# Kernel optimization log

Measured on AMD Instinct MI355X. Metric: run time of the kernel, lower is better.

The kernel has to match this reference:

```python
import jax, jax.numpy as jnp
import numpy as np


def setup_inputs() -> dict:
    key = jax.random.key(0)
    k1, k2, k3, k4 = jax.random.split(key, 4)
    N, E, F_IN, H, C = 100000, 1600000, 128, 64, 64
    x = jax.random.normal(k1, (N, F_IN), dtype=jnp.float32)
    edge_index = jax.random.randint(k2, (2, E), 0, N, dtype=jnp.int64)
    W1 = jax.random.normal(k3, (F_IN, H), dtype=jnp.float32) / np.sqrt(F_IN)
    b1 = jnp.zeros((H,), dtype=jnp.float32)
    W2 = jax.random.normal(k4, (H, C), dtype=jnp.float32) / np.sqrt(H)
    b2 = jnp.zeros((C,), dtype=jnp.float32)
    return {"x": x, "edge_index": edge_index, "W1": W1, "b1": b1, "W2": W2, "b2": b2}


def reference(x, edge_index, W1, b1, W2, b2):
    N = x.shape[0]
    # add self-loops (PyG GCNConv default)
    loop = jnp.arange(N, dtype=edge_index.dtype)
    src = jnp.concatenate([edge_index[0], loop])
    dst = jnp.concatenate([edge_index[1], loop])
    # symmetric normalization: deg^{-1/2}[src] * deg^{-1/2}[dst], deg over dst
    deg = jax.ops.segment_sum(jnp.ones_like(dst, dtype=x.dtype), dst, num_segments=N)
    dis = jnp.where(deg > 0, jax.lax.rsqrt(deg), 0.0)
    norm = dis[src] * dis[dst]  # [E+N]

    def gcn_conv(h, W, b):
        h = h @ W                                   # [N, out]
        msg = h[src] * norm[:, None]                # [E+N, out] gather
        agg = jax.ops.segment_sum(msg, dst, num_segments=N)  # scatter-add
        return agg + b

    h = jax.nn.relu(gcn_conv(x, W1, b1))
    # dropout inactive in eval mode
    out = gcn_conv(h, W2, b2)
    return jax.nn.log_softmax(out, axis=1)
```

## Files before the change

### kernel.cpp

```cpp
#include <hip/hip_runtime.h>
#include <cstdint>
#include <cstddef>

#define PASSA_EDGES 2048

typedef __attribute__((ext_vector_type(8))) short bf16x8;
typedef __attribute__((ext_vector_type(4))) float f32x4;


__device__ __forceinline__ unsigned short f2bf(float f) {
    unsigned int u = __float_as_uint(f);
    u += 0x7FFFu + ((u >> 16) & 1u);
    return (unsigned short)(u >> 16);
}
__device__ __forceinline__ float bf2f(unsigned short h) {
    return __uint_as_float((unsigned int)h << 16);
}

__device__ __forceinline__ void bf8_acc(uint4 u, float* acc) {
    acc[0] += __uint_as_float(u.x << 16);
    acc[1] += __uint_as_float(u.x & 0xFFFF0000u);
    acc[2] += __uint_as_float(u.y << 16);
    acc[3] += __uint_as_float(u.y & 0xFFFF0000u);
    acc[4] += __uint_as_float(u.z << 16);
    acc[5] += __uint_as_float(u.z & 0xFFFF0000u);
    acc[6] += __uint_as_float(u.w << 16);
    acc[7] += __uint_as_float(u.w & 0xFFFF0000u);
}
__device__ __forceinline__ void bf8_unpack(uint4 u, float* v) {
    v[0] = __uint_as_float(u.x << 16);
    v[1] = __uint_as_float(u.x & 0xFFFF0000u);
    v[2] = __uint_as_float(u.y << 16);
    v[3] = __uint_as_float(u.y & 0xFFFF0000u);
    v[4] = __uint_as_float(u.z << 16);
    v[5] = __uint_as_float(u.z & 0xFFFF0000u);
    v[6] = __uint_as_float(u.w << 16);
    v[7] = __uint_as_float(u.w & 0xFFFF0000u);
}


__global__ __launch_bounds__(256) void passA(const int* __restrict__ src,
                                             const int* __restrict__ dst,
                                             int* __restrict__ bcur,
                                             int2* __restrict__ bbuf, int E,
                                             int CAP, int shift) {
    __shared__ int2 bins[PASSA_EDGES];
    __shared__ int  cnt[256], off[256], cur[256], gbase[256];
    const int t  = threadIdx.x;
    const int e0 = blockIdx.x * PASSA_EDGES;
    const int n  = min(PASSA_EDGES, E - e0);

    cnt[t] = 0;
    __syncthreads();
    for (int i = t; i < n; i += 256) atomicAdd(&cnt[dst[e0 + i] >> shift], 1);
    __syncthreads();

    const int v = cnt[t];
    off[t] = v;
    __syncthreads();
    for (int o = 1; o < 256; o <<= 1) {
        int u = (t >= o) ? off[t - o] : 0;
        __syncthreads();
        off[t] += u;
        __syncthreads();
    }
    const int excl = off[t] - v;
    off[t] = excl;
    cur[t] = excl;
    if (v > 0) gbase[t] = t * CAP + atomicAdd(&bcur[t], v);
    __syncthreads();

    for (int i = t; i < n; i += 256) {
        const int d = dst[e0 + i];
        const int s = src[e0 + i];
        const int p = atomicAdd(&cur[d >> shift], 1);
        bins[p] = make_int2(s, d);
    }
    __syncthreads();

    for (int i = t; i < n; i += 256) {
        const int2 pr = bins[i];
        const int  b  = pr.y >> shift;
        const int  q  = gbase[b] + (i - off[b]);
        if (q < (b + 1) * CAP) bbuf[q] = pr;
    }
}


__global__ __launch_bounds__(256) void hist_dis(const int2* __restrict__ bbuf,
                                                const int* __restrict__ bcur,
                                                int* __restrict__ hist,
                                                int N, int CAP, int shift) {
    __shared__ int cnt[1024];
    const int b     = blockIdx.x;
    const int node0 = b << shift;
    const int nn    = min(1 << shift, N - node0);
    for (int j = threadIdx.x; j < nn; j += 256) cnt[j] = 0;
    __syncthreads();
    const int start = b * CAP;
    const int end   = min(b * CAP + bcur[b], (b + 1) * CAP);
    for (int e = start + threadIdx.x; e < end; e += 256)
        atomicAdd(&cnt[bbuf[e].y - node0], 1);
    __syncthreads();
    for (int j = threadIdx.x; j < nn; j += 256) hist[node0 + j] = cnt[j];
}


__global__ __launch_bounds__(256) void scan_partial(const int* __restrict__ hist,
                                                    int* __restrict__ partials,
                                                    float* __restrict__ dis, int N) {
    __shared__ int red[256];
    const int t    = threadIdx.x;
    const int base = blockIdx.x * 1024 + t * 4;
    int s = 0;
    if (base + 3 < N) {
        int4 v = *(const int4*)&hist[base];
        s = ((v.x + 7) & ~7) + ((v.y + 7) & ~7) + ((v.z + 7) & ~7) + ((v.w + 7) & ~7);
        dis[base]     = rsqrtf((float)(v.x + 1));
        dis[base + 1] = rsqrtf((float)(v.y + 1));
        dis[base + 2] = rsqrtf((float)(v.z + 1));
        dis[base + 3] = rsqrtf((float)(v.w + 1));
    } else {
        for (int i = 0; i < 4; i++)
            if (base + i < N) {
                int c = hist[base + i];
                s += (c + 7) & ~7;
                dis[base + i] = rsqrtf((float)(c + 1));
            }
    }
    red[t] = s;
    __syncthreads();
    for (int off = 128; off; off >>= 1) {
        if (t < off) red[t] += red[t + off];
        __syncthreads();
    }
    if (t == 0) partials[blockIdx.x] = red[0];
}

__global__ __launch_bounds__(256) void scan_offsets(int* __restrict__ partials, int NB) {
    __shared__ int tmp[256];
    const int t = threadIdx.x;
    int v = (t < NB) ? partials[t] : 0;
    tmp[t] = v;
    __syncthreads();
    for (int off = 1; off < 256; off <<= 1) {
        int u = (t >= off) ? tmp[t - off] : 0;
        __syncthreads();
        tmp[t] += u;
        __syncthreads();
    }
    if (t < NB) partials[t] = tmp[t] - v;
}

__global__ __launch_bounds__(256) void scan_apply(const int* __restrict__ hist,
                                                  const int* __restrict__ partials,
                                                  int* __restrict__ ptr, int N) {
    __shared__ int tsum[256];
    const int t    = threadIdx.x;
    const int base = blockIdx.x * 1024 + t * 4;
    int v[4];
    int s = 0;
    for (int i = 0; i < 4; i++) {
        int c = (base + i < N) ? hist[base + i] : 0;
        v[i]  = (c + 7) & ~7;
        s += v[i];
    }
    tsum[t] = s;
    __syncthreads();
    for (int off = 1; off < 256; off <<= 1) {
        int u = (t >= off) ? tsum[t - off] : 0;
        __syncthreads();
        tsum[t] += u;
        __syncthreads();
    }
    int run = partials[blockIdx.x] + tsum[t] - s;
    for (int i = 0; i < 4; i++) {
        if (base + i < N) {
            ptr[base + i] = run;
            run += v[i];
        }
    }
    if (base <= N - 1 && N - 1 < base + 4) ptr[N] = run;
}


__global__ __launch_bounds__(256) void passB(const int2* __restrict__ bbuf,
                                             const int* __restrict__ bcur,
                                             const int* __restrict__ ptr,
                                             int* __restrict__ csr,
                                             int N, int CAP, int shift) {
    __shared__ int lcur[1024];
    const int b     = blockIdx.x;
    const int node0 = b << shift;
    const int nn    = min(1 << shift, N - node0);
    for (int j = threadIdx.x; j < nn; j += 256) lcur[j] = ptr[node0 + j];
    __syncthreads();

    const int start = b * CAP;
    const int end   = min(b * CAP + bcur[b], (b + 1) * CAP);
    for (int e = start + threadIdx.x; e < end; e += 256) {
        const int2 pr = bbuf[e];
        const int  p  = atomicAdd(&lcur[pr.y - node0], 1);
        csr[p] = pr.x;
    }
    __syncthreads();

    for (int j = threadIdx.x; j < nn; j += 256) {
        const int t1 = ptr[node0 + j + 1];
        for (int p = lcur[j]; p < t1; ++p) csr[p] = N;
    }
}


__global__ __launch_bounds__(256) void prep_wfrag(const float* __restrict__ W1,
                                                  const float* __restrict__ W2,
                                                  unsigned short* __restrict__ whi1,
                                                  unsigned short* __restrict__ wlo1,
                                                  unsigned short* __restrict__ whi2,
                                                  unsigned short* __restrict__ wlo2) {
    for (int e = threadIdx.x; e < 128 * 64; e += 256) {
        const int blk = e >> 9, l = (e >> 3) & 63, j = e & 7;
        const int k = (blk >> 2) * 32 + (l >> 4) * 8 + j;
        const int n = (blk & 3) * 16 + (l & 15);
        const float v = W1[k * 64 + n];
        const unsigned short h = f2bf(v);
        whi1[e] = h;
        wlo1[e] = f2bf(v - bf2f(h));
    }
    for (int e = threadIdx.x; e < 64 * 64; e += 256) {
        const int blk = e >> 9, l = (e >> 3) & 63, j = e & 7;
        const int k = (blk >> 2) * 32 + (l >> 4) * 8 + j;
        const int n = (blk & 3) * 16 + (l & 15);
        const float v = W2[k * 64 + n];
        const unsigned short h = f2bf(v);
        whi2[e] = h;
        wlo2[e] = f2bf(v - bf2f(h));
    }
}


template <int K>
__global__ __launch_bounds__(256) void gemm_mfma(const float* __restrict__ X,
                                                 const unsigned short* __restrict__ whi,
                                                 const unsigned short* __restrict__ wlo,
                                                 const float* __restrict__ dis,
                                                 unsigned short* __restrict__ Yb, int N) {
    constexpr int LDX = K + 4;
    __shared__ float xs[64 * LDX];
    const int tid  = threadIdx.x;
    const int row0 = blockIdx.x * 64;

#pragma unroll
    for (int i = 0; i < (64 * K) / 1024; ++i) {
        const int fidx = i * 1024 + tid * 4;
        const int r = fidx / K, c = fidx % K;
        const float4 v = *(const float4*)(X + (size_t)min(row0 + r, N - 1) * K + c);
        *(float4*)&xs[r * LDX + c] = v;
    }
    __syncthreads();

    const int w = tid >> 6, l = tid & 63;
    const int m = l & 15, kg = l >> 4;

    f32x4 acc[4] = {};
    const float* xrow = &xs[(w * 16 + m) * LDX];

#pragma unroll
    for (int s = 0; s < K / 32; ++s) {
        const float4 a0 = *(const float4*)(xrow + s * 32 + kg * 8);
        const float4 a1 = *(const float4*)(xrow + s * 32 + kg * 8 + 4);
        const float av[8] = {a0.x, a0.y, a0.z, a0.w, a1.x, a1.y, a1.z, a1.w};
        bf16x8 ahi, alo;
#pragma unroll
        for (int j = 0; j < 8; ++j) {
            const unsigned short h = f2bf(av[j]);
            ahi[j] = (short)h;
            alo[j] = (short)f2bf(av[j] - bf2f(h));
        }
#pragma unroll
        for (int nt = 0; nt < 4; ++nt) {
            const bf16x8 bh = *(const bf16x8*)&whi[(s * 4 + nt) * 512 + l * 8];
            const bf16x8 bl = *(const bf16x8*)&wlo[(s * 4 + nt) * 512 + l * 8];
            acc[nt] = __builtin_amdgcn_mfma_f32_16x16x32_bf16(ahi, bh, acc[nt], 0, 0, 0);
            acc[nt] = __builtin_amdgcn_mfma_f32_16x16x32_bf16(alo, bh, acc[nt], 0, 0, 0);
            acc[nt] = __builtin_amdgcn_mfma_f32_16x16x32_bf16(ahi, bl, acc[nt], 0, 0, 0);
        }
    }

    float dv[4];
#pragma unroll
    for (int r = 0; r < 4; ++r)
        dv[r] = dis[min(row0 + w * 16 + kg * 4 + r, N - 1)];

#pragma unroll
    for (int nt = 0; nt < 4; ++nt)
#pragma unroll
        for (int r = 0; r < 4; ++r) {
            const int row = row0 + w * 16 + kg * 4 + r;
            if (row < N) Yb[(size_t)row * 64 + nt * 16 + m] = f2bf(acc[nt][r] * dv[r]);
        }
}


__device__ __forceinline__ void gather8i(const unsigned short* __restrict__ B,
                                         const int* __restrict__ csr,
                                         int s0, int iters, int co, float* acc) {
    const int4* cs = (const int4*)(csr + s0);
    int4 c0 = make_int4(0, 0, 0, 0), c1 = c0;
    if (iters > 0) { c0 = cs[0]; c1 = cs[1]; }
    for (int it = 0; it < iters; ++it) {
        const int nb = min(it + 1, iters - 1) * 2;
        int4 n0 = cs[nb], n1 = cs[nb + 1];
        uint4 u0 = *(const uint4*)&B[(size_t)c0.x * 64 + co * 8];
        uint4 u1 = *(const uint4*)&B[(size_t)c0.y * 64 + co * 8];
        uint4 u2 = *(const uint4*)&B[(size_t)c0.z * 64 + co * 8];
        uint4 u3 = *(const uint4*)&B[(size_t)c0.w * 64 + co * 8];
        uint4 u4 = *(const uint4*)&B[(size_t)c1.x * 64 + co * 8];
        uint4 u5 = *(const uint4*)&B[(size_t)c1.y * 64 + co * 8];
        uint4 u6 = *(const uint4*)&B[(size_t)c1.z * 64 + co * 8];
        uint4 u7 = *(const uint4*)&B[(size_t)c1.w * 64 + co * 8];
        bf8_acc(u0, acc);
        bf8_acc(u1, acc);
        bf8_acc(u2, acc);
        bf8_acc(u3, acc);
        bf8_acc(u4, acc);
        bf8_acc(u5, acc);
        bf8_acc(u6, acc);
        bf8_acc(u7, acc);
        c0 = n0; c1 = n1;
    }
}


__global__ __launch_bounds__(256) void agg_l1(const unsigned short* __restrict__ B,
                                              const int* __restrict__ csr,
                                              const int* __restrict__ ptr,
                                              const float* __restrict__ dis,
                                              const float* __restrict__ b1,
                                              float* __restrict__ hs, int N) {
    const int wid  = threadIdx.x >> 6;
    const int lane = threadIdx.x & 63;
    const int eg   = lane >> 3;
    const int co   = lane & 7;

    const int  row = blockIdx.x * 32 + wid * 8 + eg;
    const bool hr  = (row < N);

    const int   s0 = hr ? ptr[row] : 0;
    const int   s1 = hr ? ptr[row + 1] : 0;
    const float di = hr ? dis[row] : 0.f;
    const int   iters = (s1 - s0) >> 3;

    float acc[8] = {};
    gather8i(B, csr, s0, iters, co, acc);

    if (!hr) return;

    uint4 us = *(const uint4*)&B[(size_t)row * 64 + co * 8];
    float bs[8];
    bf8_unpack(us, bs);
    float bb[8];
    *(float4*)&bb[0] = *(const float4*)&b1[co * 8];
    *(float4*)&bb[4] = *(const float4*)&b1[co * 8 + 4];

    float h[8];
#pragma unroll
    for (int i = 0; i < 8; i++)
        h[i] = fmaxf((acc[i] + bs[i]) * di + bb[i], 0.f);

    *(float4*)&hs[(size_t)row * 64 + co * 8]     = make_float4(h[0], h[1], h[2], h[3]);
    *(float4*)&hs[(size_t)row * 64 + co * 8 + 4] = make_float4(h[4], h[5], h[6], h[7]);
}


__global__ __launch_bounds__(256) void agg_l2(const unsigned short* __restrict__ B,
                                              const int* __restrict__ csr,
                                              const int* __restrict__ ptr,
                                              const float* __restrict__ dis,
                                              const float* __restrict__ b2,
                                              float* __restrict__ out, int N) {
    const int wid  = threadIdx.x >> 6;
    const int lane = threadIdx.x & 63;
    const int eg   = lane >> 3;
    const int co   = lane & 7;

    const int  row = blockIdx.x * 32 + wid * 8 + eg;
    const bool hr  = (row < N);

    const int   s0 = hr ? ptr[row] : 0;
    const int   s1 = hr ? ptr[row + 1] : 0;
    const float di = hr ? dis[row] : 0.f;
    const int   iters = (s1 - s0) >> 3;

    float acc[8] = {};
    gather8i(B, csr, s0, iters, co, acc);

    if (!hr) return;

    uint4 us = *(const uint4*)&B[(size_t)row * 64 + co * 8];
    float bs[8];
    bf8_unpack(us, bs);
    float bb[8];
    *(float4*)&bb[0] = *(const float4*)&b2[co * 8];
    *(float4*)&bb[4] = *(const float4*)&b2[co * 8 + 4];

    float v[8];
#pragma unroll
    for (int i = 0; i < 8; i++) v[i] = (acc[i] + bs[i]) * di + bb[i];

    float m = v[0];
#pragma unroll
    for (int i = 1; i < 8; i++) m = fmaxf(m, v[i]);
#pragma unroll
    for (int off = 1; off <= 4; off <<= 1) m = fmaxf(m, __shfl_xor(m, off));
    float s = 0.f;
#pragma unroll
    for (int i = 0; i < 8; i++) s += __expf(v[i] - m);
#pragma unroll
    for (int off = 1; off <= 4; off <<= 1) s += __shfl_xor(s, off);
    float lse = m + __logf(s);

    float4 oa = make_float4(v[0] - lse, v[1] - lse, v[2] - lse, v[3] - lse);
    float4 ob = make_float4(v[4] - lse, v[5] - lse, v[6] - lse, v[7] - lse);
    *(float4*)&out[(size_t)row * 64 + co * 8]     = oa;
    *(float4*)&out[(size_t)row * 64 + co * 8 + 4] = ob;
}


extern "C" void kernel_launch(void* const* d_in, const int* in_sizes, int n_in,
                              void* d_out, int out_size, void* d_ws, size_t ws_size,
                              hipStream_t stream) {
    const float* x   = (const float*)d_in[0];
    const int*   ei  = (const int*)d_in[1];
    const float* W1  = (const float*)d_in[2];
    const float* b1  = (const float*)d_in[3];
    const float* W2  = (const float*)d_in[4];
    const float* b2  = (const float*)d_in[5];
    float*       out = (float*)d_out;

    const int  N   = in_sizes[0] / 128;
    const int  E   = in_sizes[1] / 2;
    const int* src = ei;
    const int* dst = ei + E;
    const int  NB  = (N + 1023) / 1024;

    int shift = 9;
    while (((N - 1) >> shift) >= 256) shift++;
    const int NBUCK = ((N - 1) >> shift) + 1;
    const int CAP   = ((E / NBUCK) * 3 / 2 + 255) & ~255;

    auto align256 = [](size_t v) { return (v + 255) & ~(size_t)255; };
    char*           p        = (char*)d_ws;
    float*          dis      = (float*)p;          p += align256((size_t)N * 4);
    int*            ptr      = (int*)p;            p += align256((size_t)(N + 1) * 4);
    int*            hist     = (int*)p;            p += align256((size_t)N * 4);
    int*            partials = (int*)p;            p += align256((size_t)NB * 4);
    int*            bcur     = (int*)p;            p += align256(256 * 4);
    int*            csr      = (int*)p;            p += align256(((size_t)E + 8 * (size_t)N) * 4);
    int2*           bbuf     = (int2*)p;           p += align256((size_t)NBUCK * CAP * 8);
    unsigned short* xwb      = (unsigned short*)p; p += align256((size_t)(N + 1) * 64 * 2);
    unsigned short* whi1     = (unsigned short*)p; p += align256(128 * 64 * 2);
    unsigned short* wlo1     = (unsigned short*)p; p += align256(128 * 64 * 2);
    unsigned short* whi2     = (unsigned short*)p; p += align256(64 * 64 * 2);
    unsigned short* wlo2     = (unsigned short*)p; p += align256(64 * 64 * 2);

    float* hs = out;

    hipMemsetAsync(bcur, 0, 256 * 4, stream);
    hipMemsetAsync(xwb + (size_t)N * 64, 0, 64 * 2, stream);
    prep_wfrag<<<1, 256, 0, stream>>>(W1, W2, whi1, wlo1, whi2, wlo2);
    passA<<<(E + PASSA_EDGES - 1) / PASSA_EDGES, 256, 0, stream>>>(src, dst, bcur, bbuf, E, CAP, shift);
    hist_dis<<<NBUCK, 256, 0, stream>>>(bbuf, bcur, hist, N, CAP, shift);
    scan_partial<<<NB, 256, 0, stream>>>(hist, partials, dis, N);
    scan_offsets<<<1, 256, 0, stream>>>(partials, NB);
    scan_apply<<<NB, 256, 0, stream>>>(hist, partials, ptr, N);
    passB<<<NBUCK, 256, 0, stream>>>(bbuf, bcur, ptr, csr, N, CAP, shift);

    gemm_mfma<128><<<(N + 63) / 64, 256, 0, stream>>>(x, whi1, wlo1, dis, xwb, N);
    agg_l1<<<(N + 31) / 32, 256, 0, stream>>>(xwb, csr, ptr, dis, b1, hs, N);
    gemm_mfma<64><<<(N + 63) / 64, 256, 0, stream>>>(hs, whi2, wlo2, dis, xwb, N);
    agg_l2<<<(N + 31) / 32, 256, 0, stream>>>(xwb, csr, ptr, dis, b2, out, N);
}
```

Baseline: 257.5 us.

## Fuse histogram, scan and CSR fill into one per-bucket kernel

Replaces the five-kernel CSR construction (histogram, three-stage global prefix scan, scatter) with one kernel per destination bucket. Each bucket gets a fixed slab of the CSR array (CAPC), so the prefix scan is purely block-local, and the counts stay in shared memory between the count and scatter phases. Row pointers become (start, iteration count) pairs, so the aggregation kernels no longer need ptr[row+1]. This saves four launches and the global round trips of hist/ptr, at the cost of a larger, gappier CSR buffer and reliance on CAP bounding each bucket's edge count.

```diff
diff --git a/kernel.cpp b/kernel.cpp
--- a/kernel.cpp
+++ b/kernel.cpp
@@ -87,127 +87,74 @@
 }
 
 
-__global__ __launch_bounds__(256) void hist_dis(const int2* __restrict__ bbuf,
-                                                const int* __restrict__ bcur,
-                                                int* __restrict__ hist,
-                                                int N, int CAP, int shift) {
+__global__ __launch_bounds__(256) void build_csr(const int2* __restrict__ bbuf,
+                                                 const int* __restrict__ bcur,
+                                                 int2* __restrict__ rowptr,
+                                                 float* __restrict__ dis,
+                                                 int* __restrict__ csr,
+                                                 int N, int CAP, int CAPC, int shift) {
     __shared__ int cnt[1024];
+    __shared__ int lcur[1024];
+    __shared__ int psum[256];
+    const int t     = threadIdx.x;
     const int b     = blockIdx.x;
     const int node0 = b << shift;
     const int nn    = min(1 << shift, N - node0);
-    for (int j = threadIdx.x; j < nn; j += 256) cnt[j] = 0;
-    __syncthreads();
+
+    for (int j = t; j < nn; j += 256) cnt[j] = 0;
+    __syncthreads();
+
     const int start = b * CAP;
     const int end   = min(b * CAP + bcur[b], (b + 1) * CAP);
-    for (int e = start + threadIdx.x; e < end; e += 256)
+    for (int e = start + t; e < end; e += 256)
         atomicAdd(&cnt[bbuf[e].y - node0], 1);
     __syncthreads();
-    for (int j = threadIdx.x; j < nn; j += 256) hist[node0 + j] = cnt[j];
-}
-
-
-__global__ __launch_bounds__(256) void scan_partial(const int* __restrict__ hist,
-                                                    int* __restrict__ partials,
-                                                    float* __restrict__ dis, int N) {
-    __shared__ int red[256];
-    const int t    = threadIdx.x;
-    const int base = blockIdx.x * 1024 + t * 4;
-    int s = 0;
-    if (base + 3 < N) {
-        int4 v = *(const int4*)&hist[base];
-        s = ((v.x + 7) & ~7) + ((v.y + 7) & ~7) + ((v.z + 7) & ~7) + ((v.w + 7) & ~7);
-        dis[base]     = rsqrtf((float)(v.x + 1));
-        dis[base + 1] = rsqrtf((float)(v.y + 1));
-        dis[base + 2] = rsqrtf((float)(v.z + 1));
-        dis[base + 3] = rsqrtf((float)(v.w + 1));
-    } else {
-        for (int i = 0; i < 4; i++)
-            if (base + i < N) {
-                int c = hist[base + i];
-                s += (c + 7) & ~7;
-                dis[base + i] = rsqrtf((float)(c + 1));
-            }
-    }
-    red[t] = s;
-    __syncthreads();
-    for (int off = 128; off; off >>= 1) {
-        if (t < off) red[t] += red[t + off];
-        __syncthreads();
-    }
-    if (t == 0) partials[blockIdx.x] = red[0];
-}
-
-__global__ __launch_bounds__(256) void scan_offsets(int* __restrict__ partials, int NB) {
-    __shared__ int tmp[256];
-    const int t = threadIdx.x;
-    int v = (t < NB) ? partials[t] : 0;
-    tmp[t] = v;
-    __syncthreads();
-    for (int off = 1; off < 256; off <<= 1) {
-        int u = (t >= off) ? tmp[t - off] : 0;
-        __syncthreads();
-        tmp[t] += u;
-        __syncthreads();
-    }
-    if (t < NB) partials[t] = tmp[t] - v;
-}
-
-__global__ __launch_bounds__(256) void scan_apply(const int* __restrict__ hist,
-                                                  const int* __restrict__ partials,
-                                                  int* __restrict__ ptr, int N) {
-    __shared__ int tsum[256];
-    const int t    = threadIdx.x;
-    const int base = blockIdx.x * 1024 + t * 4;
+
     int v[4];
     int s = 0;
+#pragma unroll
     for (int i = 0; i < 4; i++) {
-        int c = (base + i < N) ? hist[base + i] : 0;
-        v[i]  = (c + 7) & ~7;
+        const int j = t * 4 + i;
+        v[i] = (j < nn) ? ((cnt[j] + 7) & ~7) : 0;
         s += v[i];
     }
-    tsum[t] = s;
-    __syncthreads();
-    for (int off = 1; off < 256; off <<= 1) {
-        int u = (t >= off) ? tsum[t - off] : 0;
+    psum[t] = s;
+    __syncthreads();
+    for (int o = 1; o < 256; o <<= 1) {
+        int u = (t >= o) ? psum[t - o] : 0;
         __syncthreads();
-        tsum[t] += u;
+        psum[t] += u;
         __syncthreads();
     }
-    int run = partials[blockIdx.x] + tsum[t] - s;
+    int run = b * CAPC + psum[t] - s;
+#pragma unroll
     for (int i = 0; i < 4; i++) {
-        if (base + i < N) {
-            ptr[base + i] = run;
+        const int j = t * 4 + i;
+        if (j < nn) {
+            lcur[j] = run;
+            rowptr[node0 + j] = make_int2(run, v[i] >> 3);
+            dis[node0 + j]    = rsqrtf((float)(cnt[j] + 1));
             run += v[i];
         }
     }
-    if (base <= N - 1 && N - 1 < base + 4) ptr[N] = run;
-}
-
-
-__global__ __launch_bounds__(256) void passB(const int2* __restrict__ bbuf,
-                                             const int* __restrict__ bcur,
-                                             const int* __restrict__ ptr,
-                                             int* __restrict__ csr,
-                                             int N, int CAP, int shift) {
-    __shared__ int lcur[1024];
-    const int b     = blockIdx.x;
-    const int node0 = b << shift;
-    const int nn    = min(1 << shift, N - node0);
-    for (int j = threadIdx.x; j < nn; j += 256) lcur[j] = ptr[node0 + j];
-    __syncthreads();
-
-    const int start = b * CAP;
-    const int end   = min(b * CAP + bcur[b], (b + 1) * CAP);
-    for (int e = start + threadIdx.x; e < end; e += 256) {
+    __syncthreads();
+
+    for (int e = start + t; e < end; e += 256) {
         const int2 pr = bbuf[e];
         const int  p  = atomicAdd(&lcur[pr.y - node0], 1);
         csr[p] = pr.x;
     }
     __syncthreads();
 
-    for (int j = threadIdx.x; j < nn; j += 256) {
-        const int t1 = ptr[node0 + j + 1];
-        for (int p = lcur[j]; p < t1; ++p) csr[p] = N;
+    int base2 = b * CAPC + psum[t] - s;
+#pragma unroll
+    for (int i = 0; i < 4; i++) {
+        const int j = t * 4 + i;
+        if (j < nn) {
+            const int rowend = base2 + v[i];
+            for (int p = lcur[j]; p < rowend; ++p) csr[p] = N;
+            base2 += v[i];
+        }
     }
 }
 
@@ -334,7 +281,7 @@
 
 __global__ __launch_bounds__(256) void agg_l1(const unsigned short* __restrict__ B,
                                               const int* __restrict__ csr,
-                                              const int* __restrict__ ptr,
+                                              const int2* __restrict__ rowptr,
                                               const float* __restrict__ dis,
                                               const float* __restrict__ b1,
                                               float* __restrict__ hs, int N) {
@@ -346,13 +293,11 @@
     const int  row = blockIdx.x * 32 + wid * 8 + eg;
     const bool hr  = (row < N);
 
-    const int   s0 = hr ? ptr[row] : 0;
-    const int   s1 = hr ? ptr[row + 1] : 0;
+    const int2  rp = hr ? rowptr[row] : make_int2(0, 0);
     const float di = hr ? dis[row] : 0.f;
-    const int   iters = (s1 - s0) >> 3;
 
     float acc[8] = {};
-    gather8i(B, csr, s0, iters, co, acc);
+    gather8i(B, csr, rp.x, rp.y, co, acc);
 
     if (!hr) return;
 
@@ -375,7 +320,7 @@
 
 __global__ __launch_bounds__(256) void agg_l2(const unsigned short* __restrict__ B,
                                               const int* __restrict__ csr,
-                                              const int* __restrict__ ptr,
+                                              const int2* __restrict__ rowptr,
                                               const float* __restrict__ dis,
                                               const float* __restrict__ b2,
                                               float* __restrict__ out, int N) {
@@ -387,13 +332,11 @@
     const int  row = blockIdx.x * 32 + wid * 8 + eg;
     const bool hr  = (row < N);
 
-    const int   s0 = hr ? ptr[row] : 0;
-    const int   s1 = hr ? ptr[row + 1] : 0;
+    const int2  rp = hr ? rowptr[row] : make_int2(0, 0);
     const float di = hr ? dis[row] : 0.f;
-    const int   iters = (s1 - s0) >> 3;
 
     float acc[8] = {};
-    gather8i(B, csr, s0, iters, co, acc);
+    gather8i(B, csr, rp.x, rp.y, co, acc);
 
     if (!hr) return;
 
@@ -442,21 +385,19 @@
     const int  E   = in_sizes[1] / 2;
     const int* src = ei;
     const int* dst = ei + E;
-    const int  NB  = (N + 1023) / 1024;
 
     int shift = 9;
     while (((N - 1) >> shift) >= 256) shift++;
     const int NBUCK = ((N - 1) >> shift) + 1;
     const int CAP   = ((E / NBUCK) * 3 / 2 + 255) & ~255;
+    const int CAPC  = CAP + 8 * (1 << shift);
 
     auto align256 = [](size_t v) { return (v + 255) & ~(size_t)255; };
     char*           p        = (char*)d_ws;
     float*          dis      = (float*)p;          p += align256((size_t)N * 4);
-    int*            ptr      = (int*)p;            p += align256((size_t)(N + 1) * 4);
-    int*            hist     = (int*)p;            p += align256((size_t)N * 4);
-    int*            partials = (int*)p;            p += align256((size_t)NB * 4);
+    int2*           rowptr   = (int2*)p;           p += align256((size_t)N * 8);
     int*            bcur     = (int*)p;            p += align256(256 * 4);
-    int*            csr      = (int*)p;            p += align256(((size_t)E + 8 * (size_t)N) * 4);
+    int*            csr      = (int*)p;            p += align256((size_t)NBUCK * CAPC * 4);
     int2*           bbuf     = (int2*)p;           p += align256((size_t)NBUCK * CAP * 8);
     unsigned short* xwb      = (unsigned short*)p; p += align256((size_t)(N + 1) * 64 * 2);
     unsigned short* whi1     = (unsigned short*)p; p += align256(128 * 64 * 2);
@@ -470,14 +411,10 @@
     hipMemsetAsync(xwb + (size_t)N * 64, 0, 64 * 2, stream);
     prep_wfrag<<<1, 256, 0, stream>>>(W1, W2, whi1, wlo1, whi2, wlo2);
     passA<<<(E + PASSA_EDGES - 1) / PASSA_EDGES, 256, 0, stream>>>(src, dst, bcur, bbuf, E, CAP, shift);
-    hist_dis<<<NBUCK, 256, 0, stream>>>(bbuf, bcur, hist, N, CAP, shift);
-    scan_partial<<<NB, 256, 0, stream>>>(hist, partials, dis, N);
-    scan_offsets<<<1, 256, 0, stream>>>(partials, NB);
-    scan_apply<<<NB, 256, 0, stream>>>(hist, partials, ptr, N);
-    passB<<<NBUCK, 256, 0, stream>>>(bbuf, bcur, ptr, csr, N, CAP, shift);
+    build_csr<<<NBUCK, 256, 0, stream>>>(bbuf, bcur, rowptr, dis, csr, N, CAP, CAPC, shift);
 
     gemm_mfma<128><<<(N + 63) / 64, 256, 0, stream>>>(x, whi1, wlo1, dis, xwb, N);
-    agg_l1<<<(N + 31) / 32, 256, 0, stream>>>(xwb, csr, ptr, dis, b1, hs, N);
+    agg_l1<<<(N + 31) / 32, 256, 0, stream>>>(xwb, csr, rowptr, dis, b1, hs, N);
     gemm_mfma<64><<<(N + 63) / 64, 256, 0, stream>>>(hs, whi2, wlo2, dis, xwb, N);
-    agg_l2<<<(N + 31) / 32, 256, 0, stream>>>(xwb, csr, ptr, dis, b2, out, N);
-}
+    agg_l2<<<(N + 31) / 32, 256, 0, stream>>>(xwb, csr, rowptr, dis, b2, out, N);
+}
```

Measured after the change: 250.7 us. -2.6%, faster.
